# Performance work log

Hardware: AMD Instinct MI355X
Metric: run time of the kernel (lower is better)

The kernel has to match this reference:

```python
import jax, jax.numpy as jnp
import numpy as np

B, N, C, H = 16, 576, 768, 12
HD = C // H
SCALE = HD ** -0.5


def setup_inputs() -> dict:
    key = jax.random.key(0)
    ks = jax.random.split(key, 8)
    s = lambda fan: 1.0 / np.sqrt(fan)
    return {
        "x": jax.random.normal(ks[0], (B, N, C), jnp.float32),
        "Wqkv": jax.random.normal(ks[1], (3 * C, C), jnp.float32) * s(C),
        "Wl": jax.random.normal(ks[2], (H, H), jnp.float32) * s(H),
        "bl": jax.random.normal(ks[3], (H,), jnp.float32) * 0.02,
        "Ww": jax.random.normal(ks[4], (H, H), jnp.float32) * s(H),
        "bw": jax.random.normal(ks[5], (H,), jnp.float32) * 0.02,
        "Wproj": jax.random.normal(ks[6], (C, C), jnp.float32) * s(C),
        "bproj": jax.random.normal(ks[7], (C,), jnp.float32) * 0.02,
    }


def reference(x, Wqkv, Wl, bl, Ww, bw, Wproj, bproj):
    b, n, c = x.shape
    # qkv projection: (B,N,3C) -> (3,B,H,N,HD)
    qkv = (x @ Wqkv.T).reshape(b, n, 3, H, HD)
    qkv = jnp.transpose(qkv, (2, 0, 3, 1, 4))
    q, k, v = qkv[0] * SCALE, qkv[1], qkv[2]
    # raw scores (B,H,N,N)
    attn = jnp.einsum("bhmd,bhnd->bhmn", q, k)
    # talking-heads pre-softmax mix over head axis (nn.Linear: y = x @ W.T + b)
    attn = jnp.einsum("bhmn,gh->bgmn", attn, Wl) + bl[None, :, None, None]
    attn = jax.nn.softmax(attn, axis=-1)
    # talking-heads post-softmax mix
    attn = jnp.einsum("bhmn,gh->bgmn", attn, Ww) + bw[None, :, None, None]
    # attn @ V -> (B,N,C)
    out = jnp.einsum("bhmn,bhnd->bhmd", attn, v)
    out = jnp.transpose(out, (0, 2, 1, 3)).reshape(b, n, c)
    return out @ Wproj.T + bproj
```

## Files before the change

### kernel.cpp

```cpp
#include <hip/hip_runtime.h>

#define B_ 16
#define N_ 576
#define C_ 768
#define H_ 12
#define HD_ 64
#define M_ (B_*N_)
#define C3_ (3*C_)
#define KC_ 3
#define NT_ 18

typedef _Float16 f16;
typedef _Float16 f16x8 __attribute__((ext_vector_type(8)));
typedef _Float16 f16x4 __attribute__((ext_vector_type(4)));
typedef float f32x4 __attribute__((ext_vector_type(4)));
typedef float f32x2 __attribute__((ext_vector_type(2)));

__global__ void cvt_f32_f16(const float* __restrict__ in, f16* __restrict__ out, int n4) {
    int i = blockIdx.x * blockDim.x + threadIdx.x;
    int stride = gridDim.x * blockDim.x;
    for (; i < n4; i += stride) {
        float4 v = ((const float4*)in)[i];
        f16x4 o = { (f16)v.x, (f16)v.y, (f16)v.z, (f16)v.w };
        ((f16x4*)out)[i] = o;
    }
}

__device__ __forceinline__ int swz(int row, int slot) {
    return row * 32 + ((slot ^ ((row >> 1) & 3)) * 8);
}

__device__ __forceinline__ void gload16(const void* g, void* l) {
    __builtin_amdgcn_global_load_lds((const __attribute__((address_space(1))) void*)g,
                                     (__attribute__((address_space(3))) void*)l, 16, 0, 0);
}

__device__ __forceinline__ size_t qk_frag_off(int bh12, int t16, int half, int l) {
    return (((size_t)bh12 * 36 + t16) * 2 + half) * 512 + (size_t)l * 8;
}

__global__ __launch_bounds__(256) void gemm_qkv(const f16* __restrict__ A, const f16* __restrict__ Bw,
                                                f16* __restrict__ Qf, f16* __restrict__ Kf, f16* __restrict__ Vo) {
    __shared__ __align__(16) f16 lA[128 * 32];
    __shared__ __align__(16) f16 lB[128 * 32];
    __shared__ __align__(16) f16 eT[4][16][72];
    const int K = C_;
    int m0 = blockIdx.x * 128, n0 = blockIdx.y * 128;
    int t = threadIdx.x, lane = t & 63, wave = t >> 6;
    int wm = (wave >> 1) * 64, wn = (wave & 1) * 64;
    int srow0 = wave * 16 + (lane >> 2);
    int scol0 = ((lane & 3) ^ ((srow0 >> 1) & 3)) * 8;
    int srow1 = srow0 + 64;
    int scol1 = ((lane & 3) ^ ((srow1 >> 1) & 3)) * 8;
    f16* dA0 = lA + wave * 512 + lane * 8;
    f16* dA1 = lA + 2048 + wave * 512 + lane * 8;
    f16* dB0 = lB + wave * 512 + lane * 8;
    f16* dB1 = lB + 2048 + wave * 512 + lane * 8;
    const f16* A0 = A + (size_t)(m0 + srow0) * K + scol0;
    const f16* A1 = A + (size_t)(m0 + srow1) * K + scol1;
    const f16* B0 = Bw + (size_t)(n0 + srow0) * K + scol0;
    const f16* B1 = Bw + (size_t)(n0 + srow1) * K + scol1;
    f32x4 acc[4][4] = {};
    for (int k0 = 0; k0 < K; k0 += 32) {
        gload16(A0 + k0, dA0);
        gload16(A1 + k0, dA1);
        gload16(B0 + k0, dB0);
        gload16(B1 + k0, dB1);
        __syncthreads();
        f16x8 af[4], bf[4];
#pragma unroll
        for (int i = 0; i < 4; ++i) {
            af[i] = *(const f16x8*)(lA + swz(wm + i * 16 + (lane & 15), lane >> 4));
            bf[i] = *(const f16x8*)(lB + swz(wn + i * 16 + (lane & 15), lane >> 4));
        }
#pragma unroll
        for (int i = 0; i < 4; ++i)
#pragma unroll
            for (int j = 0; j < 4; ++j)
                acc[i][j] = __builtin_amdgcn_mfma_f32_16x16x32_f16(af[i], bf[j], acc[i][j], 0, 0, 0);
        __syncthreads();
    }
    int colw = n0 + wn;
    int tsel = colw / C_;
    int rem = colw - tsel * C_;
    int h = rem >> 6;
    float qs = (tsel == 0) ? 0.125f : 1.0f;
#pragma unroll
    for (int i = 0; i < 4; ++i) {
        int rowg = m0 + wm + i * 16;
        int bb = rowg / N_;
        int nnb = rowg - bb * N_;
        int bh = bb * H_ + h;
#pragma unroll
        for (int j = 0; j < 4; ++j)
#pragma unroll
            for (int r = 0; r < 4; ++r)
                eT[wave][(lane >> 4) * 4 + r][j * 16 + (lane & 15)] = (f16)(acc[i][j][r] * qs);
        if (tsel < 2) {
            f16* dst = (tsel == 0) ? Qf : Kf;
#pragma unroll
            for (int half = 0; half < 2; ++half) {
                f16x8 v = *(const f16x8*)&eT[wave][lane & 15][half * 32 + (lane >> 4) * 8];
                *(f16x8*)(dst + qk_frag_off(bh, nnb >> 4, half, lane)) = v;
            }
        } else {
#pragma unroll
            for (int hh = 0; hh < 2; ++hh) {
                int nl = hh * 8 + (lane >> 3);
                f16x8 v = *(const f16x8*)&eT[wave][nl][(lane & 7) * 8];
                *(f16x8*)(Vo + ((size_t)bh * N_ + nnb + nl) * HD_ + (lane & 7) * 8) = v;
            }
        }
    }
}

__global__ __launch_bounds__(256) void gemm_proj(const f16* __restrict__ A, const f16* __restrict__ Bw,
                                                 const float* __restrict__ bias, float* __restrict__ out) {
    __shared__ __align__(16) f16 lA[128 * 32];
    __shared__ __align__(16) f16 lB[128 * 32];
    const int K = C_;
    const size_t PSZ = (size_t)M_ * C_;
    int m0 = blockIdx.x * 128, n0 = blockIdx.y * 128;
    int t = threadIdx.x, lane = t & 63, wave = t >> 6;
    int wm = (wave >> 1) * 64, wn = (wave & 1) * 64;
    int srow = t >> 2, sslot = t & 3, scol = sslot * 8;
    int brow0 = wave * 16 + (lane >> 2);
    int bcol0 = ((lane & 3) ^ ((brow0 >> 1) & 3)) * 8;
    int brow1 = brow0 + 64;
    int bcol1 = ((lane & 3) ^ ((brow1 >> 1) & 3)) * 8;
    f16* dB0 = lB + wave * 512 + lane * 8;
    f16* dB1 = lB + 2048 + wave * 512 + lane * 8;
    const f16* B0 = Bw + (size_t)(n0 + brow0) * K + bcol0;
    const f16* B1 = Bw + (size_t)(n0 + brow1) * K + bcol1;
    f32x4 acc[4][4] = {};
    for (int k0 = 0; k0 < K; k0 += 32) {
        gload16(B0 + k0, dB0);
        gload16(B1 + k0, dB1);
        {
            size_t i0 = (size_t)(m0 + srow) * K + k0 + scol;
            size_t i1 = (size_t)(m0 + srow + 64) * K + k0 + scol;
            f16x8 a0 = *(const f16x8*)(A + i0), a1 = *(const f16x8*)(A + PSZ + i0), a2 = *(const f16x8*)(A + 2 * PSZ + i0);
            *(f16x8*)(lA + swz(srow, sslot)) = a0 + a1 + a2;
            f16x8 b0 = *(const f16x8*)(A + i1), b1 = *(const f16x8*)(A + PSZ + i1), b2 = *(const f16x8*)(A + 2 * PSZ + i1);
            *(f16x8*)(lA + swz(srow + 64, sslot)) = b0 + b1 + b2;
        }
        __syncthreads();
        f16x8 af[4], bf[4];
#pragma unroll
        for (int i = 0; i < 4; ++i) {
            af[i] = *(const f16x8*)(lA + swz(wm + i * 16 + (lane & 15), lane >> 4));
            bf[i] = *(const f16x8*)(lB + swz(wn + i * 16 + (lane & 15), lane >> 4));
        }
#pragma unroll
        for (int i = 0; i < 4; ++i)
#pragma unroll
            for (int j = 0; j < 4; ++j)
                acc[i][j] = __builtin_amdgcn_mfma_f32_16x16x32_f16(af[i], bf[j], acc[i][j], 0, 0, 0);
        __syncthreads();
    }
#pragma unroll
    for (int i = 0; i < 4; ++i) {
        int row0 = m0 + wm + i * 16 + ((lane >> 4) * 4);
#pragma unroll
        for (int j = 0; j < 4; ++j) {
            int col = n0 + wn + j * 16 + (lane & 15);
            float bv = bias[col];
#pragma unroll
            for (int r = 0; r < 4; ++r)
                out[(size_t)(row0 + r) * C_ + col] = acc[i][j][r] + bv;
        }
    }
}

__global__ void transpose_v(const f16* __restrict__ V, f16* __restrict__ Vf) {
    __shared__ f16 tile[64][68];
    int bh = blockIdx.y, n0 = blockIdx.x * 64;
    const f16* src = V + (size_t)bh * N_ * HD_;
    int t = threadIdx.x;
#pragma unroll
    for (int i = 0; i < 16; ++i) {
        int e = i * 256 + t;
        int r = e >> 6, c = e & 63;
        tile[r][c] = src[(size_t)(n0 + r) * HD_ + c];
    }
    __syncthreads();
#pragma unroll
    for (int i = 0; i < 2; ++i) {
        int u = i * 256 + t;
        int nt2 = u >> 8, dt = (u >> 6) & 3, l = u & 63;
        int nl = nt2 * 32 + ((l >> 4) << 3);
        int d = dt * 16 + (l & 15);
        f16x8 v;
#pragma unroll
        for (int j = 0; j < 8; ++j) v[j] = tile[nl + j][d];
        size_t off = (((size_t)bh * 18 + (n0 >> 5) + nt2) * 4 + dt) * 512 + (size_t)l * 8;
        *(f16x8*)(Vf + off) = v;
    }
}

__global__ __launch_bounds__(512) void scores_exp(const f16* __restrict__ Qf, const f16* __restrict__ Kf,
                                                  const float* __restrict__ Wl, const float* __restrict__ bl,
                                                  unsigned char* __restrict__ Sp, float* __restrict__ rps) {
    __shared__ float sWl[144];
    __shared__ float sbl[12];
    __shared__ f16 red[12][64][2];
    __shared__ __align__(16) f16 lK[2 * 12 * 2 * 512];
    int fl = blockIdx.x;
    int xcd = fl & 7;
    int j = fl >> 3;
    int hi = (j >= 162) ? 1 : 0;
    int b = xcd * 2 + hi;
    int j2 = j - hi * 162;
    int yt = j2 / 9;
    int mb = j2 - yt * 9;
    int t = threadIdx.x, lane = t & 63, wave = t >> 6;
    int mh = wave >> 2 ? 0 : 0;
    mh = wave >> 1;
    int nh = wave & 1;
    if (t < 144) sWl[t] = Wl[t];
    if (t >= 192 && t < 204) sbl[t - 192] = bl[t - 192];
#pragma unroll
    for (int i = 0; i < 6; ++i) {
        int c = wave * 6 + i;
        int nh2 = c / 24, rest = c - nh2 * 24;
        int h = rest >> 1, half = rest & 1;
        gload16(Kf + qk_frag_off(b * H_ + h, yt * 2 + nh2, half, 0) + (size_t)lane * 8,
                lK + c * 512 + lane * 8);
    }
    __syncthreads();
    int m16 = lane & 15, q = lane >> 4;
    int mt16 = mb * 4 + mh;
    f32x4 S[12];
#pragma unroll
    for (int h = 0; h < 12; ++h) {
        int bh = b * H_ + h;
        f16x8 k0 = *(const f16x8*)(lK + ((nh * 12 + h) * 2 + 0) * 512 + lane * 8);
        f16x8 k1 = *(const f16x8*)(lK + ((nh * 12 + h) * 2 + 1) * 512 + lane * 8);
        f16x8 q0 = *(const f16x8*)(Qf + qk_frag_off(bh, mt16, 0, lane));
        f16x8 q1 = *(const f16x8*)(Qf + qk_frag_off(bh, mt16, 1, lane));
        f32x4 a = {0.f, 0.f, 0.f, 0.f};
        a = __builtin_amdgcn_mfma_f32_16x16x32_f16(k0, q0, a, 0, 0, 0);
        a = __builtin_amdgcn_mfma_f32_16x16x32_f16(k1, q1, a, 0, 0, 0);
        S[h] = a;
    }
    int oct = nh * 2 + (q >> 1);
    int lp = m16 | (oct << 4);
    int jo = (q & 1) * 4;
    unsigned char* spb = Sp + ((((size_t)b * 36 + mt16) * 18 + yt) * 12) * 512 + lp * 8 + jo;
    float sg[12];
#pragma unroll
    for (int g = 0; g < 12; ++g) {
        float bg = sbl[g];
        f32x4 w = {bg, bg, bg, bg};
#pragma unroll
        for (int h = 0; h < 12; ++h) w += sWl[g * 12 + h] * S[h];
        float e0 = __expf(w[0]), e1 = __expf(w[1]), e2 = __expf(w[2]), e3 = __expf(w[3]);
        sg[g] = e0 + e1 + e2 + e3;
        unsigned int pk = 0;
        pk = __builtin_amdgcn_cvt_pk_fp8_f32(e0 * 0.25f, e1 * 0.25f, pk, false);
        pk = __builtin_amdgcn_cvt_pk_fp8_f32(e2 * 0.25f, e3 * 0.25f, pk, true);
        *(unsigned int*)(spb + g * 512) = pk;
    }
#pragma unroll
    for (int g = 0; g < 12; ++g) {
        float v = sg[g];
        v += __shfl_xor(v, 16, 64);
        v += __shfl_xor(v, 32, 64);
        if (lane < 16) red[g][mh * 16 + lane][nh] = (f16)v;
    }
    __syncthreads();
    for (int tt = t; tt < 768; tt += 512) {
        int g = tt >> 6, mr = tt & 63;
        float tot = (float)red[g][mr][0] + (float)red[g][mr][1];
        rps[(((size_t)b * H_ + g) * N_ + mb * 64 + mr) * NT_ + yt] = tot;
    }
}

__global__ __launch_bounds__(256) void sum_rinv(const float* __restrict__ rps, float* __restrict__ rinv) {
    int row = blockIdx.x * 256 + threadIdx.x;
    const float* p = rps + (size_t)row * NT_;
    float s = 0.f;
#pragma unroll
    for (int i = 0; i < NT_; ++i) s += p[i];
    rinv[row] = 1.0f / s;
}

__global__ __launch_bounds__(256) void pv_mix(const unsigned char* __restrict__ Sp, const f16* __restrict__ Vf,
                                              const float* __restrict__ Ww, const float* __restrict__ bw,
                                              const float* __restrict__ rinv, f16* __restrict__ Opart) {
    __shared__ float ils[12][16];
    int fl = blockIdx.x;
    int sw = (fl & 7) * 216 + (fl >> 3);
    int mt = sw % 36, rem = sw / 36;
    int b = rem & 15, kc = rem >> 4;
    int m0 = mt * 16;
    int t = threadIdx.x, lane = t & 63;
    int wv = __builtin_amdgcn_readfirstlane(t >> 6);
    if (t < 192) ils[t / 16][t % 16] = rinv[((size_t)b * H_ + t / 16) * N_ + m0 + (t % 16)];
    __syncthreads();
    int mrow = lane & 15, n8 = lane >> 4;
    float il_[12];
#pragma unroll
    for (int h = 0; h < 12; ++h) il_[h] = 4.0f * ils[h][mrow];
    float ww0[12], ww1[12], ww2[12];
#pragma unroll
    for (int h = 0; h < 12; ++h) {
        ww0[h] = Ww[(wv * 3 + 0) * H_ + h];
        ww1[h] = Ww[(wv * 3 + 1) * H_ + h];
        ww2[h] = Ww[(wv * 3 + 2) * H_ + h];
    }
    float bw0 = bw[wv * 3], bw1 = bw[wv * 3 + 1], bw2 = bw[wv * 3 + 2];
    const unsigned char* spf = Sp + (((size_t)b * 36 + mt) * 18 + kc * 6) * 6144;
    const f16* vfb = Vf + ((((size_t)b * 12 + wv * 3) * 18 + kc * 6) * 4) * 512;
    f32x4 O[3][4] = {};
    for (int it = 0; it < 6; ++it) {
        uint2 ck8[12];
#pragma unroll
        for (int c = 0; c < 12; ++c)
            ck8[c] = *(const uint2*)(spf + (size_t)(it * 12 + c) * 512 + lane * 8);
        float w0[8], w1[8], w2[8];
#pragma unroll
        for (int jj = 0; jj < 8; ++jj) { w0[jj] = bw0; w1[jj] = bw1; w2[jj] = bw2; }
#pragma unroll
        for (int h = 0; h < 12; ++h) {
            float il = il_[h];
            float c0 = ww0[h], c1 = ww1[h], c2 = ww2[h];
            f32x2 eA = __builtin_amdgcn_cvt_pk_f32_fp8(ck8[h].x, false);
            f32x2 eB = __builtin_amdgcn_cvt_pk_f32_fp8(ck8[h].x, true);
            f32x2 eC = __builtin_amdgcn_cvt_pk_f32_fp8(ck8[h].y, false);
            f32x2 eD = __builtin_amdgcn_cvt_pk_f32_fp8(ck8[h].y, true);
            float p0 = eA.x * il, p1 = eA.y * il, p2 = eB.x * il, p3 = eB.y * il;
            float p4 = eC.x * il, p5 = eC.y * il, p6 = eD.x * il, p7 = eD.y * il;
            w0[0] += c0 * p0; w0[1] += c0 * p1; w0[2] += c0 * p2; w0[3] += c0 * p3;
            w0[4] += c0 * p4; w0[5] += c0 * p5; w0[6] += c0 * p6; w0[7] += c0 * p7;
            w1[0] += c1 * p0; w1[1] += c1 * p1; w1[2] += c1 * p2; w1[3] += c1 * p3;
            w1[4] += c1 * p4; w1[5] += c1 * p5; w1[6] += c1 * p6; w1[7] += c1 * p7;
            w2[0] += c2 * p0; w2[1] += c2 * p1; w2[2] += c2 * p2; w2[3] += c2 * p3;
            w2[4] += c2 * p4; w2[5] += c2 * p5; w2[6] += c2 * p6; w2[7] += c2 * p7;
        }
        f16x8 af0, af1, af2;
#pragma unroll
        for (int jj = 0; jj < 8; ++jj) {
            af0[jj] = (f16)w0[jj]; af1[jj] = (f16)w1[jj]; af2[jj] = (f16)w2[jj];
        }
#pragma unroll
        for (int dt = 0; dt < 4; ++dt) {
            f16x8 bf0 = *(const f16x8*)(vfb + (size_t)0 * 36864 + it * 2048 + dt * 512 + lane * 8);
            O[0][dt] = __builtin_amdgcn_mfma_f32_16x16x32_f16(af0, bf0, O[0][dt], 0, 0, 0);
            f16x8 bf1 = *(const f16x8*)(vfb + (size_t)1 * 36864 + it * 2048 + dt * 512 + lane * 8);
            O[1][dt] = __builtin_amdgcn_mfma_f32_16x16x32_f16(af1, bf1, O[1][dt], 0, 0, 0);
            f16x8 bf2 = *(const f16x8*)(vfb + (size_t)2 * 36864 + it * 2048 + dt * 512 + lane * 8);
            O[2][dt] = __builtin_amdgcn_mfma_f32_16x16x32_f16(af2, bf2, O[2][dt], 0, 0, 0);
        }
    }
    f16* Ob = Opart + (size_t)kc * M_ * C_;
#pragma unroll
    for (int gi = 0; gi < 3; ++gi) {
        int g = wv * 3 + gi;
#pragma unroll
        for (int dt = 0; dt < 4; ++dt)
#pragma unroll
            for (int r = 0; r < 4; ++r)
                Ob[((size_t)b * N_ + m0 + n8 * 4 + r) * C_ + g * HD_ + dt * 16 + mrow] = (f16)O[gi][dt][r];
    }
}

extern "C" void kernel_launch(void* const* d_in, const int* in_sizes, int n_in,
                              void* d_out, int out_size, void* d_ws, size_t ws_size,
                              hipStream_t stream) {
    const float* x     = (const float*)d_in[0];
    const float* Wqkv  = (const float*)d_in[1];
    const float* Wl    = (const float*)d_in[2];
    const float* bl    = (const float*)d_in[3];
    const float* Ww    = (const float*)d_in[4];
    const float* bw    = (const float*)d_in[5];
    const float* Wproj = (const float*)d_in[6];
    const float* bproj = (const float*)d_in[7];
    float* out = (float*)d_out;

    char* ws = (char*)d_ws;
    size_t off = 0;
    auto alloc = [&](size_t bytes) -> void* {
        void* p = ws + off;
        off += (bytes + 255) & ~(size_t)255;
        return p;
    };
    f16* x_h  = (f16*)alloc((size_t)M_ * C_ * 2);
    f16* wq_h = (f16*)alloc((size_t)C3_ * C_ * 2);
    f16* wp_h = (f16*)alloc((size_t)C_ * C_ * 2);
    f16* qf_h = (f16*)alloc((size_t)B_ * H_ * N_ * HD_ * 2);
    f16* kf_h = (f16*)alloc((size_t)B_ * H_ * N_ * HD_ * 2);
    f16* v_h  = (f16*)alloc((size_t)B_ * H_ * N_ * HD_ * 2);
    f16* vf_h = (f16*)alloc((size_t)B_ * H_ * N_ * HD_ * 2);
    unsigned char* sp = (unsigned char*)alloc((size_t)B_ * N_ * N_ * 12);
    float* rps  = (float*)alloc((size_t)B_ * H_ * N_ * NT_ * 4);
    float* rinv = (float*)alloc((size_t)B_ * H_ * N_ * 4);
    f16* opart = (f16*)alloc((size_t)KC_ * M_ * C_ * 2);

    cvt_f32_f16<<<1024, 256, 0, stream>>>(x,     x_h,  M_ * C_ / 4);
    cvt_f32_f16<<<1024, 256, 0, stream>>>(Wqkv,  wq_h, C3_ * C_ / 4);
    cvt_f32_f16<<<512,  256, 0, stream>>>(Wproj, wp_h, C_ * C_ / 4);

    gemm_qkv<<<dim3(M_ / 128, C3_ / 128), 256, 0, stream>>>(x_h, wq_h, qf_h, kf_h, v_h);
    transpose_v<<<dim3(N_ / 64, B_ * H_), 256, 0, stream>>>(v_h, vf_h);
    scores_exp<<<2592, 512, 0, stream>>>(qf_h, kf_h, Wl, bl, sp, rps);
    sum_rinv<<<(B_ * H_ * N_) / 256, 256, 0, stream>>>(rps, rinv);
    pv_mix<<<36 * 16 * KC_, 256, 0, stream>>>(sp, vf_h, Ww, bw, rinv, opart);
    gemm_proj<<<dim3(M_ / 128, C_ / 128), 256, 0, stream>>>(opart, wp_h, bproj, out);
}
```

Baseline: 202.6 us.

## Split scores_exp into 256-thread blocks, drop LDS reduction, use packed FMA head mix

```diff
diff --git a/kernel.cpp b/kernel.cpp
--- a/kernel.cpp
+++ b/kernel.cpp
@@ -8,7 +8,8 @@
 #define M_ (B_*N_)
 #define C3_ (3*C_)
 #define KC_ 3
-#define NT_ 18
+#define NT_ 36
+#define BHN_ (B_*H_*N_)
 
 typedef _Float16 f16;
 typedef _Float16 f16x8 __attribute__((ext_vector_type(8)));
@@ -38,6 +39,19 @@
 __device__ __forceinline__ size_t qk_frag_off(int bh12, int t16, int half, int l) {
     return (((size_t)bh12 * 36 + t16) * 2 + half) * 512 + (size_t)l * 8;
 }
+
+__device__ __forceinline__ f32x2 pkfma_lo(f32x2 a, f32x2 b, f32x2 c) {
+    asm("v_pk_fma_f32 %0, %1, %2, %0 op_sel:[0,0,0] op_sel_hi:[0,1,1]"
+        : "+v"(c) : "v"(a), "v"(b));
+    return c;
+}
+__device__ __forceinline__ f32x2 pkfma_hi(f32x2 a, f32x2 b, f32x2 c) {
+    asm("v_pk_fma_f32 %0, %1, %2, %0 op_sel:[1,0,0] op_sel_hi:[1,1,1]"
+        : "+v"(c) : "v"(a), "v"(b));
+    return c;
+}
+__device__ __forceinline__ f32x2 vlo(f32x4 v) { return __builtin_shufflevector(v, v, 0, 1); }
+__device__ __forceinline__ f32x2 vhi(f32x4 v) { return __builtin_shufflevector(v, v, 2, 3); }
 
 __global__ __launch_bounds__(256) void gemm_qkv(const f16* __restrict__ A, const f16* __restrict__ Bw,
                                                 f16* __restrict__ Qf, f16* __restrict__ Kf, f16* __restrict__ Vo) {
@@ -198,44 +212,39 @@
     }
 }
 
-__global__ __launch_bounds__(512) void scores_exp(const f16* __restrict__ Qf, const f16* __restrict__ Kf,
+__global__ __launch_bounds__(256) void scores_exp(const f16* __restrict__ Qf, const f16* __restrict__ Kf,
                                                   const float* __restrict__ Wl, const float* __restrict__ bl,
                                                   unsigned char* __restrict__ Sp, float* __restrict__ rps) {
-    __shared__ float sWl[144];
+    __shared__ __align__(8) float sWl[144];
     __shared__ float sbl[12];
-    __shared__ f16 red[12][64][2];
-    __shared__ __align__(16) f16 lK[2 * 12 * 2 * 512];
+    __shared__ __align__(16) f16 lK[12 * 2 * 512];
     int fl = blockIdx.x;
     int xcd = fl & 7;
     int j = fl >> 3;
-    int hi = (j >= 162) ? 1 : 0;
+    int hi = (j >= 324) ? 1 : 0;
     int b = xcd * 2 + hi;
-    int j2 = j - hi * 162;
+    int j2 = j - hi * 324;
     int yt = j2 / 9;
     int mb = j2 - yt * 9;
     int t = threadIdx.x, lane = t & 63, wave = t >> 6;
-    int mh = wave >> 2 ? 0 : 0;
-    mh = wave >> 1;
-    int nh = wave & 1;
     if (t < 144) sWl[t] = Wl[t];
     if (t >= 192 && t < 204) sbl[t - 192] = bl[t - 192];
 #pragma unroll
     for (int i = 0; i < 6; ++i) {
         int c = wave * 6 + i;
-        int nh2 = c / 24, rest = c - nh2 * 24;
-        int h = rest >> 1, half = rest & 1;
-        gload16(Kf + qk_frag_off(b * H_ + h, yt * 2 + nh2, half, 0) + (size_t)lane * 8,
+        int h = c >> 1, half = c & 1;
+        gload16(Kf + qk_frag_off(b * H_ + h, yt, half, 0) + (size_t)lane * 8,
                 lK + c * 512 + lane * 8);
     }
     __syncthreads();
     int m16 = lane & 15, q = lane >> 4;
-    int mt16 = mb * 4 + mh;
+    int mt16 = mb * 4 + wave;
     f32x4 S[12];
 #pragma unroll
     for (int h = 0; h < 12; ++h) {
         int bh = b * H_ + h;
-        f16x8 k0 = *(const f16x8*)(lK + ((nh * 12 + h) * 2 + 0) * 512 + lane * 8);
-        f16x8 k1 = *(const f16x8*)(lK + ((nh * 12 + h) * 2 + 1) * 512 + lane * 8);
+        f16x8 k0 = *(const f16x8*)(lK + (h * 2 + 0) * 512 + lane * 8);
+        f16x8 k1 = *(const f16x8*)(lK + (h * 2 + 1) * 512 + lane * 8);
         f16x8 q0 = *(const f16x8*)(Qf + qk_frag_off(bh, mt16, 0, lane));
         f16x8 q1 = *(const f16x8*)(Qf + qk_frag_off(bh, mt16, 1, lane));
         f32x4 a = {0.f, 0.f, 0.f, 0.f};
@@ -243,18 +252,24 @@
         a = __builtin_amdgcn_mfma_f32_16x16x32_f16(k1, q1, a, 0, 0, 0);
         S[h] = a;
     }
-    int oct = nh * 2 + (q >> 1);
+    int oct = (yt & 1) * 2 + (q >> 1);
     int lp = m16 | (oct << 4);
     int jo = (q & 1) * 4;
-    unsigned char* spb = Sp + ((((size_t)b * 36 + mt16) * 18 + yt) * 12) * 512 + lp * 8 + jo;
+    unsigned char* spb = Sp + ((((size_t)b * 36 + mt16) * 18 + (yt >> 1)) * 12) * 512 + lp * 8 + jo;
     float sg[12];
 #pragma unroll
     for (int g = 0; g < 12; ++g) {
         float bg = sbl[g];
-        f32x4 w = {bg, bg, bg, bg};
-#pragma unroll
-        for (int h = 0; h < 12; ++h) w += sWl[g * 12 + h] * S[h];
-        float e0 = __expf(w[0]), e1 = __expf(w[1]), e2 = __expf(w[2]), e3 = __expf(w[3]);
+        f32x2 w01 = {bg, bg}, w23 = {bg, bg};
+#pragma unroll
+        for (int hp = 0; hp < 6; ++hp) {
+            f32x2 wlp = *(const f32x2*)&sWl[g * 12 + hp * 2];
+            w01 = pkfma_lo(wlp, vlo(S[hp * 2]), w01);
+            w23 = pkfma_lo(wlp, vhi(S[hp * 2]), w23);
+            w01 = pkfma_hi(wlp, vlo(S[hp * 2 + 1]), w01);
+            w23 = pkfma_hi(wlp, vhi(S[hp * 2 + 1]), w23);
+        }
+        float e0 = __expf(w01.x), e1 = __expf(w01.y), e2 = __expf(w23.x), e3 = __expf(w23.y);
         sg[g] = e0 + e1 + e2 + e3;
         unsigned int pk = 0;
         pk = __builtin_amdgcn_cvt_pk_fp8_f32(e0 * 0.25f, e1 * 0.25f, pk, false);
@@ -266,22 +281,18 @@
         float v = sg[g];
         v += __shfl_xor(v, 16, 64);
         v += __shfl_xor(v, 32, 64);
-        if (lane < 16) red[g][mh * 16 + lane][nh] = (f16)v;
-    }
-    __syncthreads();
-    for (int tt = t; tt < 768; tt += 512) {
-        int g = tt >> 6, mr = tt & 63;
-        float tot = (float)red[g][mr][0] + (float)red[g][mr][1];
-        rps[(((size_t)b * H_ + g) * N_ + mb * 64 + mr) * NT_ + yt] = tot;
+        if (lane < 16) {
+            int row = (b * H_ + g) * N_ + mb * 64 + wave * 16 + m16;
+            rps[(size_t)yt * BHN_ + row] = v;
+        }
     }
 }
 
 __global__ __launch_bounds__(256) void sum_rinv(const float* __restrict__ rps, float* __restrict__ rinv) {
     int row = blockIdx.x * 256 + threadIdx.x;
-    const float* p = rps + (size_t)row * NT_;
     float s = 0.f;
 #pragma unroll
-    for (int i = 0; i < NT_; ++i) s += p[i];
+    for (int i = 0; i < NT_; ++i) s += rps[(size_t)i * BHN_ + row];
     rinv[row] = 1.0f / s;
 }
 
@@ -393,8 +404,8 @@
     f16* v_h  = (f16*)alloc((size_t)B_ * H_ * N_ * HD_ * 2);
     f16* vf_h = (f16*)alloc((size_t)B_ * H_ * N_ * HD_ * 2);
     unsigned char* sp = (unsigned char*)alloc((size_t)B_ * N_ * N_ * 12);
-    float* rps  = (float*)alloc((size_t)B_ * H_ * N_ * NT_ * 4);
-    float* rinv = (float*)alloc((size_t)B_ * H_ * N_ * 4);
+    float* rps  = (float*)alloc((size_t)NT_ * BHN_ * 4);
+    float* rinv = (float*)alloc((size_t)BHN_ * 4);
     f16* opart = (f16*)alloc((size_t)KC_ * M_ * C_ * 2);
 
     cvt_f32_f16<<<1024, 256, 0, stream>>>(x,     x_h,  M_ * C_ / 4);
@@ -403,8 +414,8 @@
 
     gemm_qkv<<<dim3(M_ / 128, C3_ / 128), 256, 0, stream>>>(x_h, wq_h, qf_h, kf_h, v_h);
     transpose_v<<<dim3(N_ / 64, B_ * H_), 256, 0, stream>>>(v_h, vf_h);
-    scores_exp<<<2592, 512, 0, stream>>>(qf_h, kf_h, Wl, bl, sp, rps);
-    sum_rinv<<<(B_ * H_ * N_) / 256, 256, 0, stream>>>(rps, rinv);
+    scores_exp<<<5184, 256, 0, stream>>>(qf_h, kf_h, Wl, bl, sp, rps);
+    sum_rinv<<<BHN_ / 256, 256, 0, stream>>>(rps, rinv);
     pv_mix<<<36 * 16 * KC_, 256, 0, stream>>>(sp, vf_h, Ww, bw, rinv, opart);
     gemm_proj<<<dim3(M_ / 128, C_ / 128), 256, 0, stream>>>(opart, wp_h, bproj, out);
 }
```

After: 199.3 us, median of 2. About the same (-1.6%).
